# Kernel optimization log

Hardware: AMD Instinct MI355X
Metric: run time of the kernel (lower is better)

## Reference

```python
import jax, jax.numpy as jnp
import numpy as np

RANK = 200
N_ENT = 200_000
N_REL = 500
NNZ = 500_000


def setup_inputs() -> dict:
    key = jax.random.key(0)
    k1, k2, k3, k4, k5 = jax.random.split(key, 5)
    # xavier_normal_ init: std = sqrt(2 / (fan_in + fan_out))
    a = jax.random.normal(k1, (N_ENT, RANK), dtype=jnp.float32) * np.float32(np.sqrt(2.0 / (N_ENT + RANK)))
    b = jax.random.normal(k2, (N_REL, RANK), dtype=jnp.float32) * np.float32(np.sqrt(2.0 / (N_REL + RANK)))
    subj = jax.random.randint(k3, (NNZ,), 0, N_ENT)
    rel = jax.random.randint(k4, (NNZ,), 0, N_REL)
    obj = jax.random.randint(k5, (NNZ,), 0, N_ENT)
    coo_ns = jnp.stack([subj, rel, obj], axis=1)  # [nnz, 3]
    vals_ns = jnp.ones((NNZ,), dtype=jnp.float32)  # observed tensor values (positives)
    return {"coo_ns": coo_ns, "vals_ns": vals_ns, "a": a, "b": b}


def reference(coo_ns, vals_ns, a, b):
    # Gather factor rows for each nonzero coordinate (irregular gather)
    a0 = a[coo_ns[:, 0], :]  # [nnz, R] subject entity rows
    b1 = b[coo_ns[:, 1], :]  # [nnz, R] relation rows
    a2 = a[coo_ns[:, 2], :]  # [nnz, R] object entity rows

    # Khatri-Rao style elementwise product + rank reduction
    kruskal_val = jnp.sum(a0 * b1 * a2, axis=1)  # [nnz]

    # squared-error GCP loss and its derivative w.r.t. kruskal_val
    diff = kruskal_val - vals_ns
    loss = diff * diff                 # [nnz]
    deriv = 2.0 * diff                 # [nnz]

    # per-nonzero MTTKRP gradient rows (mttcrp1 with same-coordinate trick)
    g_a = deriv[:, None] * b1 * a2     # mode 0
    g_b = deriv[:, None] * a0 * a2     # mode 1
    g_c = deriv[:, None] * a0 * b1     # mode 2

    # scatter (overwrite, as in a_torch.grad[a_elems,:] = g_a etc.)
    grad_a = jnp.zeros_like(a).at[coo_ns[:, 0]].set(g_a).at[coo_ns[:, 2]].set(g_c)
    grad_b = jnp.zeros_like(b).at[coo_ns[:, 1]].set(g_b)
    return loss, grad_a, grad_b
```

## Files before the change

### kernel.cpp

```cpp
#include <hip/hip_runtime.h>
#include <hip/hip_bf16.h>

#define RANK   200
#define N_ENT  200000
#define N_REL  500
#define NNZ    500000
#define NB_WIN 256
#define WB_PAD 512

__global__ void winner_kernel(const int* __restrict__ coo,
                              int* __restrict__ wA,
                              int* __restrict__ partial_wB) {
    __shared__ int lwB[WB_PAD];
    for (int t = threadIdx.x; t < WB_PAD; t += blockDim.x) lwB[t] = -1;
    __syncthreads();

    int gtid   = blockIdx.x * blockDim.x + threadIdx.x;
    int stride = gridDim.x * blockDim.x;
    for (int i = gtid; i < NNZ; i += stride) {
        int s = coo[3 * i + 0];
        int r = coo[3 * i + 1];
        int o = coo[3 * i + 2];
        atomicMax(&wA[s], i);
        atomicMax(&wA[o], NNZ + i);
        atomicMax(&lwB[r], i);
    }
    __syncthreads();
    int* out = partial_wB + (size_t)blockIdx.x * WB_PAD;
    for (int t = threadIdx.x; t < WB_PAD; t += blockDim.x) out[t] = lwB[t];
}

__global__ void wb_reduce_kernel(const int* __restrict__ partial_wB,
                                 int* __restrict__ wB) {
    int t = threadIdx.x;
    int m = -1;
    for (int nb = 0; nb < NB_WIN; ++nb)
        m = max(m, partial_wB[(size_t)nb * WB_PAD + t]);
    if (t < N_REL) wB[t] = m;
}

__global__ void loss_kernel(const int* __restrict__ coo,
                            const float* __restrict__ vals,
                            const float* __restrict__ a,
                            const float* __restrict__ b,
                            float* __restrict__ loss,
                            float* __restrict__ diff) {
    int wave = (blockIdx.x * blockDim.x + threadIdx.x) >> 6;
    int lane = threadIdx.x & 63;
    if (wave >= NNZ) return;
    int s = coo[3 * wave + 0];
    int r = coo[3 * wave + 1];
    int o = coo[3 * wave + 2];
    float sum = 0.0f;
    if (lane < RANK / 4) {
        const float4* as_ = (const float4*)(a + (size_t)s * RANK) + lane;
        const float4* br_ = (const float4*)(b + (size_t)r * RANK) + lane;
        const float4* ao_ = (const float4*)(a + (size_t)o * RANK) + lane;
        float4 x = *as_, y = *br_, z = *ao_;
        sum = x.x * y.x * z.x + x.y * y.y * z.y
            + x.z * y.z * z.z + x.w * y.w * z.w;
    }
    #pragma unroll
    for (int off = 32; off > 0; off >>= 1)
        sum += __shfl_down(sum, off, 64);
    if (lane == 0) {
        float d = sum - vals[wave];
        loss[wave] = d * d;
        diff[wave] = d;
    }
}

__global__ void grad_kernel(const int* __restrict__ coo,
                            const float* __restrict__ diff,
                            const float* __restrict__ a,
                            const float* __restrict__ b,
                            const int* __restrict__ wA,
                            const int* __restrict__ wB,
                            float* __restrict__ grad_a,
                            float* __restrict__ grad_b) {
    int row  = (blockIdx.x * blockDim.x + threadIdx.x) >> 6;
    int lane = threadIdx.x & 63;
    if (row >= N_ENT + N_REL) return;

    const float *x, *y;
    float d = 0.0f;
    float4* out;
    if (row < N_ENT) {
        out = (float4*)(grad_a + (size_t)row * RANK);
        int key = wA[row];
        if (key < 0) {
            if (lane < RANK / 4) out[lane] = make_float4(0.f, 0.f, 0.f, 0.f);
            return;
        }
        bool is_obj = key >= NNZ;
        int i = is_obj ? (key - NNZ) : key;
        int s = coo[3 * i + 0];
        int r = coo[3 * i + 1];
        int o = coo[3 * i + 2];
        d = 2.0f * diff[i];
        x = b + (size_t)r * RANK;
        y = is_obj ? (a + (size_t)s * RANK)
                   : (a + (size_t)o * RANK);
    } else {
        int rr = row - N_ENT;
        out = (float4*)(grad_b + (size_t)rr * RANK);
        int key = wB[rr];
        if (key < 0) {
            if (lane < RANK / 4) out[lane] = make_float4(0.f, 0.f, 0.f, 0.f);
            return;
        }
        int s = coo[3 * key + 0];
        int o = coo[3 * key + 2];
        d = 2.0f * diff[key];
        x = a + (size_t)s * RANK;
        y = a + (size_t)o * RANK;
    }
    if (lane < RANK / 4) {
        float4 xv = ((const float4*)x)[lane];
        float4 yv = ((const float4*)y)[lane];
        out[lane] = make_float4(d * xv.x * yv.x, d * xv.y * yv.y,
                                d * xv.z * yv.z, d * xv.w * yv.w);
    }
}

extern "C" void kernel_launch(void* const* d_in, const int* in_sizes, int n_in,
                              void* d_out, int out_size, void* d_ws, size_t ws_size,
                              hipStream_t stream) {
    const int*   coo  = (const int*)d_in[0];
    const float* vals = (const float*)d_in[1];
    const float* a    = (const float*)d_in[2];
    const float* b    = (const float*)d_in[3];

    float* loss   = (float*)d_out;
    float* grad_a = loss + NNZ;
    float* grad_b = grad_a + (size_t)N_ENT * RANK;

    float* diff       = (float*)d_ws;
    int*   wA         = (int*)(diff + NNZ);
    int*   wB         = wA + N_ENT;
    int*   partial_wB = wB + WB_PAD;

    hipMemsetAsync(wA, 0xFF, (size_t)N_ENT * sizeof(int), stream);

    winner_kernel<<<NB_WIN, 256, 0, stream>>>(coo, wA, partial_wB);
    wb_reduce_kernel<<<1, WB_PAD, 0, stream>>>(partial_wB, wB);
    {
        long long total = (long long)NNZ * 64;
        int threads = 256;
        long long blocks = (total + threads - 1) / threads;
        loss_kernel<<<(int)blocks, threads, 0, stream>>>(coo, vals, a, b, loss, diff);
    }
    {
        long long total = (long long)(N_ENT + N_REL) * 64;
        int threads = 256;
        long long blocks = (total + threads - 1) / threads;
        grad_kernel<<<(int)blocks, threads, 0, stream>>>(coo, diff, a, b, wA, wB,
                                                         grad_a, grad_b);
    }
}
```

Before: 479.9 us.

## Fuse gradient writes into loss kernel and zero untouched rows separately

The loss kernel now also writes the winning gradient rows directly. Each nonzero checks whether it is the last writer for its subject, object and relation rows, and reuses the factor rows already held in registers. This removes the separate grad kernel, which re-gathered coo, diff and factor rows for every entity, and drops the diff workspace. A new compact kernel zeroes only the rows nobody wrote, using ballot to pack one row per wave iteration. The cost is extra winner-table lookups per nonzero and uncoalesced scattered writes inside the fused kernel.

```diff
diff --git a/kernel.cpp b/kernel.cpp
--- a/kernel.cpp
+++ b/kernel.cpp
@@ -39,87 +39,84 @@
     if (t < N_REL) wB[t] = m;
 }
 
-__global__ void loss_kernel(const int* __restrict__ coo,
-                            const float* __restrict__ vals,
-                            const float* __restrict__ a,
-                            const float* __restrict__ b,
-                            float* __restrict__ loss,
-                            float* __restrict__ diff) {
+__global__ void fused_kernel(const int* __restrict__ coo,
+                             const float* __restrict__ vals,
+                             const float* __restrict__ a,
+                             const float* __restrict__ b,
+                             const int* __restrict__ wA,
+                             const int* __restrict__ wB,
+                             float* __restrict__ loss,
+                             float* __restrict__ grad_a,
+                             float* __restrict__ grad_b) {
     int wave = (blockIdx.x * blockDim.x + threadIdx.x) >> 6;
     int lane = threadIdx.x & 63;
     if (wave >= NNZ) return;
     int s = coo[3 * wave + 0];
     int r = coo[3 * wave + 1];
     int o = coo[3 * wave + 2];
+    int ks = wA[s];
+    int ko = wA[o];
+    int kr = wB[r];
+
+    float4 x = make_float4(0.f, 0.f, 0.f, 0.f);
+    float4 y = x, z = x;
     float sum = 0.0f;
     if (lane < RANK / 4) {
-        const float4* as_ = (const float4*)(a + (size_t)s * RANK) + lane;
-        const float4* br_ = (const float4*)(b + (size_t)r * RANK) + lane;
-        const float4* ao_ = (const float4*)(a + (size_t)o * RANK) + lane;
-        float4 x = *as_, y = *br_, z = *ao_;
+        x = ((const float4*)(a + (size_t)s * RANK))[lane];
+        y = ((const float4*)(b + (size_t)r * RANK))[lane];
+        z = ((const float4*)(a + (size_t)o * RANK))[lane];
         sum = x.x * y.x * z.x + x.y * y.y * z.y
             + x.z * y.z * z.z + x.w * y.w * z.w;
     }
     #pragma unroll
     for (int off = 32; off > 0; off >>= 1)
-        sum += __shfl_down(sum, off, 64);
-    if (lane == 0) {
-        float d = sum - vals[wave];
-        loss[wave] = d * d;
-        diff[wave] = d;
+        sum += __shfl_xor(sum, off, 64);
+
+    float d = sum - vals[wave];
+    if (lane == 0) loss[wave] = d * d;
+    float d2 = 2.0f * d;
+
+    if (lane < RANK / 4) {
+        if (ks == wave) {
+            float4* outp = (float4*)(grad_a + (size_t)s * RANK);
+            outp[lane] = make_float4(d2 * y.x * z.x, d2 * y.y * z.y,
+                                     d2 * y.z * z.z, d2 * y.w * z.w);
+        }
+        if (ko == NNZ + wave) {
+            float4* outp = (float4*)(grad_a + (size_t)o * RANK);
+            outp[lane] = make_float4(d2 * x.x * y.x, d2 * x.y * y.y,
+                                     d2 * x.z * y.z, d2 * x.w * y.w);
+        }
+        if (kr == wave) {
+            float4* outp = (float4*)(grad_b + (size_t)r * RANK);
+            outp[lane] = make_float4(d2 * x.x * z.x, d2 * x.y * z.y,
+                                     d2 * x.z * z.z, d2 * x.w * z.w);
+        }
     }
 }
 
-__global__ void grad_kernel(const int* __restrict__ coo,
-                            const float* __restrict__ diff,
-                            const float* __restrict__ a,
-                            const float* __restrict__ b,
-                            const int* __restrict__ wA,
-                            const int* __restrict__ wB,
-                            float* __restrict__ grad_a,
-                            float* __restrict__ grad_b) {
-    int row  = (blockIdx.x * blockDim.x + threadIdx.x) >> 6;
+__global__ void zero_untouched_kernel(const int* __restrict__ wA,
+                                      const int* __restrict__ wB,
+                                      float* __restrict__ grad_a,
+                                      float* __restrict__ grad_b) {
+    int tid  = blockIdx.x * blockDim.x + threadIdx.x;
     int lane = threadIdx.x & 63;
-    if (row >= N_ENT + N_REL) return;
-
-    const float *x, *y;
-    float d = 0.0f;
-    float4* out;
-    if (row < N_ENT) {
-        out = (float4*)(grad_a + (size_t)row * RANK);
-        int key = wA[row];
-        if (key < 0) {
-            if (lane < RANK / 4) out[lane] = make_float4(0.f, 0.f, 0.f, 0.f);
-            return;
-        }
-        bool is_obj = key >= NNZ;
-        int i = is_obj ? (key - NNZ) : key;
-        int s = coo[3 * i + 0];
-        int r = coo[3 * i + 1];
-        int o = coo[3 * i + 2];
-        d = 2.0f * diff[i];
-        x = b + (size_t)r * RANK;
-        y = is_obj ? (a + (size_t)s * RANK)
-                   : (a + (size_t)o * RANK);
-    } else {
-        int rr = row - N_ENT;
-        out = (float4*)(grad_b + (size_t)rr * RANK);
-        int key = wB[rr];
-        if (key < 0) {
-            if (lane < RANK / 4) out[lane] = make_float4(0.f, 0.f, 0.f, 0.f);
-            return;
-        }
-        int s = coo[3 * key + 0];
-        int o = coo[3 * key + 2];
-        d = 2.0f * diff[key];
-        x = a + (size_t)s * RANK;
-        y = a + (size_t)o * RANK;
+    bool need = false;
+    if (tid < N_ENT) {
+        need = (wA[tid] < 0);
+    } else if (tid < N_ENT + N_REL) {
+        need = (wB[tid - N_ENT] < 0);
     }
-    if (lane < RANK / 4) {
-        float4 xv = ((const float4*)x)[lane];
-        float4 yv = ((const float4*)y)[lane];
-        out[lane] = make_float4(d * xv.x * yv.x, d * xv.y * yv.y,
-                                d * xv.z * yv.z, d * xv.w * yv.w);
+    unsigned long long mask = __ballot(need);
+    while (mask) {
+        int src = __ffsll((long long)mask) - 1;
+        mask &= mask - 1;
+        int rowsel = __shfl(tid, src, 64);
+        float4* outp = (rowsel < N_ENT)
+            ? (float4*)(grad_a + (size_t)rowsel * RANK)
+            : (float4*)(grad_b + (size_t)(rowsel - N_ENT) * RANK);
+        if (lane < RANK / 4)
+            outp[lane] = make_float4(0.f, 0.f, 0.f, 0.f);
     }
 }
 
@@ -135,10 +132,9 @@
     float* grad_a = loss + NNZ;
     float* grad_b = grad_a + (size_t)N_ENT * RANK;
 
-    float* diff       = (float*)d_ws;
-    int*   wA         = (int*)(diff + NNZ);
-    int*   wB         = wA + N_ENT;
-    int*   partial_wB = wB + WB_PAD;
+    int* wA         = (int*)d_ws;
+    int* wB         = wA + N_ENT;
+    int* partial_wB = wB + WB_PAD;
 
     hipMemsetAsync(wA, 0xFF, (size_t)N_ENT * sizeof(int), stream);
 
@@ -148,13 +144,13 @@
         long long total = (long long)NNZ * 64;
         int threads = 256;
         long long blocks = (total + threads - 1) / threads;
-        loss_kernel<<<(int)blocks, threads, 0, stream>>>(coo, vals, a, b, loss, diff);
+        fused_kernel<<<(int)blocks, threads, 0, stream>>>(coo, vals, a, b, wA, wB,
+                                                          loss, grad_a, grad_b);
     }
     {
-        long long total = (long long)(N_ENT + N_REL) * 64;
+        int total   = N_ENT + N_REL;
         int threads = 256;
-        long long blocks = (total + threads - 1) / threads;
-        grad_kernel<<<(int)blocks, threads, 0, stream>>>(coo, diff, a, b, wA, wB,
-                                                         grad_a, grad_b);
+        int blocks  = (total + threads - 1) / threads;
+        zero_untouched_kernel<<<blocks, threads, 0, stream>>>(wA, wB, grad_a, grad_b);
     }
 }
```

New measurement: 460.8 us. -4.0%, faster.
